# Performance work log

Hardware: AMD Instinct MI355X
Metric: run time of the kernel (lower is better)

Reference implementation:

```python
import jax, jax.numpy as jnp
import numpy as np

N_NODE = 100000
N_EDGE = 1000000
HID = 64
ATTN = 32
N_REL = 1000
N_LAYER = 2
REL_VOCAB = 2 * N_REL + 5


def setup_inputs() -> dict:
    key = jax.random.key(0)
    ks = jax.random.split(key, 16)
    sub = jax.random.randint(ks[0], (N_EDGE,), 0, N_NODE)
    rel = jax.random.randint(ks[1], (N_EDGE,), 0, REL_VOCAB)
    obj = jax.random.randint(ks[2], (N_EDGE,), 0, N_NODE)
    zero = jnp.zeros((N_EDGE,), dtype=jnp.int64 if jax.config.jax_enable_x64 else jnp.int32)
    # columns: [_, _, rel, _, sub, obj] matching edges[:,2]/[:,4]/[:,5]
    edges = jnp.stack([zero, zero, rel, zero, sub, obj], axis=1)
    s = 0.05
    return {
        "edges": edges,
        "rela_embed": jax.random.normal(ks[3], (N_LAYER, REL_VOCAB, HID), jnp.float32) * s,
        "Ws": jax.random.normal(ks[4], (N_LAYER, ATTN, HID), jnp.float32) * s,
        "Wr": jax.random.normal(ks[5], (N_LAYER, ATTN, HID), jnp.float32) * s,
        "w_alpha_w": jax.random.normal(ks[6], (N_LAYER, 1, ATTN), jnp.float32) * s,
        "w_alpha_b": jax.random.normal(ks[7], (N_LAYER, 1), jnp.float32) * s,
        "W_h": jax.random.normal(ks[8], (N_LAYER, HID, HID), jnp.float32) * s,
        "gru_Wih": jax.random.normal(ks[9], (N_LAYER, 3 * HID, HID), jnp.float32) * s,
        "gru_Whh": jax.random.normal(ks[10], (N_LAYER, 3 * HID, HID), jnp.float32) * s,
        "gru_bih": jax.random.normal(ks[11], (N_LAYER, 3 * HID), jnp.float32) * s,
        "gru_bhh": jax.random.normal(ks[12], (N_LAYER, 3 * HID), jnp.float32) * s,
        "W_final": jax.random.normal(ks[13], (HID,), jnp.float32) * s,
    }


def _gru_cell(x, h, Wih, Whh, bih, bhh):
    # PyTorch nn.GRU single step; gate order: r, z, n
    gi = x @ Wih.T + bih          # [N, 3H]
    gh = h @ Whh.T + bhh          # [N, 3H]
    gi_r, gi_z, gi_n = jnp.split(gi, 3, axis=-1)
    gh_r, gh_z, gh_n = jnp.split(gh, 3, axis=-1)
    r = jax.nn.sigmoid(gi_r + gh_r)
    z = jax.nn.sigmoid(gi_z + gh_z)
    n = jnp.tanh(gi_n + r * gh_n)
    return (1.0 - z) * n + z * h


def reference(edges, rela_embed, Ws, Wr, w_alpha_w, w_alpha_b, W_h,
              gru_Wih, gru_Whh, gru_bih, gru_bhh, W_final):
    sub = edges[:, 4]
    rel = edges[:, 2]
    obj = edges[:, 5]
    hidden = jnp.zeros((N_NODE, HID), jnp.float32)
    h0 = jnp.zeros((N_NODE, HID), jnp.float32)
    for i in range(N_LAYER):
        hs = hidden[sub]                          # [E, H] gather
        hr = rela_embed[i][rel]                   # [E, H] gather
        # attention: sigmoid(w_alpha(relu(Ws hs + Wr hr)))
        a = jax.nn.relu(hs @ Ws[i].T + hr @ Wr[i].T)       # [E, A]
        alpha = jax.nn.sigmoid(a @ w_alpha_w[i].T + w_alpha_b[i])  # [E, 1]
        message = alpha * (hs + hr)               # [E, H]
        agg = jax.ops.segment_sum(message, obj, num_segments=N_NODE)  # [N, H]
        hidden = jax.nn.relu(agg @ W_h[i].T)       # act = relu
        # dropout is identity in eval; GRU gate (seq len 1)
        h = _gru_cell(hidden, h0, gru_Wih[i], gru_Whh[i], gru_bih[i], gru_bhh[i])
        hidden = h
        h0 = h
    scores = hidden @ W_final                      # [N_NODE]
    return scores
```

## Files before the change

kernel.cpp:

```cpp
#include <hip/hip_runtime.h>

#define N_NODE 100000
#define N_PAD  100064
#define N_EDGE 1000000
#define HID 64
#define ATTN 32
#define REL_VOCAB 2005

#define CBSHIFT 9
#define CBN    512
#define NCB    196
#define MAXCB  8192
#define LCAP   6400
#define N_SLOT (NCB*MAXCB)
#define ACHUNK 4096

typedef short  bf16x8 __attribute__((ext_vector_type(8)));
typedef float  f32x4  __attribute__((ext_vector_type(4)));

__device__ __forceinline__ float sigf(float x){ return 1.0f/(1.0f+__expf(-x)); }
__device__ __forceinline__ float bf2f(unsigned short u){
  return __uint_as_float(((unsigned int)u) << 16);
}
__device__ __forceinline__ unsigned short f2bf(float f){
  unsigned int x = __float_as_uint(f);
  x += 0x7fffu + ((x >> 16) & 1u);
  return (unsigned short)(x >> 16);
}

__device__ __forceinline__ float dot64(const float4* a, const float4* __restrict__ w){
  float s0=0.f,s1=0.f,s2=0.f,s3=0.f;
  #pragma unroll
  for (int i=0;i<16;i++){
    float4 av=a[i]; float4 wv=w[i];
    s0=fmaf(av.x,wv.x,s0); s1=fmaf(av.y,wv.y,s1);
    s2=fmaf(av.z,wv.z,s2); s3=fmaf(av.w,wv.w,s3);
  }
  return (s0+s1)+(s2+s3);
}

__global__ void __launch_bounds__(256, 4) k_pre(
    const float* __restrict__ re, const float* __restrict__ Wr,
    const float* __restrict__ ww, const float* __restrict__ wb,
    unsigned short* __restrict__ srel16, unsigned short* __restrict__ re16,
    float* __restrict__ hrW1)
{
  int w = (blockIdx.x*blockDim.x + threadIdx.x) >> 6;
  int l = threadIdx.x & 63;
  if (w >= REL_VOCAB) return;
  const int r = w;
  const int j = l & 31;
  const bool hi = (l >= 32);

  float4 ev[16];
  const float4* ep = (const float4*)(re + (size_t)(hi ? REL_VOCAB + r : r)*HID);
  #pragma unroll
  for (int i=0;i<16;i++) ev[i]=ep[i];

  const float4* wrow = (const float4*)(Wr + (size_t)(hi ? ATTN + j : j)*HID);
  float d = dot64(ev, wrow);

  if (hi) hrW1[r*ATTN + j] = d;

  float p = hi ? 0.f : fmaxf(d, 0.f) * ww[j];
  p += __shfl_xor(p, 1);
  p += __shfl_xor(p, 2);
  p += __shfl_xor(p, 4);
  p += __shfl_xor(p, 8);
  p += __shfl_xor(p, 16);
  p += __shfl_xor(p, 32);
  float alpha = sigf(p + wb[0]);

  float e0l = re[(size_t)r*HID + l];
  float e1l = re[(size_t)(REL_VOCAB + r)*HID + l];
  srel16[r*HID + l] = f2bf(alpha * e0l);
  re16[r*HID + l]   = f2bf(e1l);
}

__global__ void k_izero(int* __restrict__ p, int n){
  int i = blockIdx.x*blockDim.x + threadIdx.x;
  if (i < n) p[i] = 0;
}

__global__ void k_wt(const float* __restrict__ Wh, const float* __restrict__ Wih,
                     const float* __restrict__ Whh, const float* __restrict__ Ws,
                     unsigned short* __restrict__ pkWh, unsigned short* __restrict__ pkWih,
                     unsigned short* __restrict__ pkWhh, unsigned short* __restrict__ pkWs)
{
  int tid = blockIdx.x*blockDim.x + threadIdx.x;
  if (tid >= 116*64) return;
  int rec = tid >> 6, l = tid & 63;
  const float* src; unsigned short* dst; int tile, c;
  if (rec < 16){
    int li = rec >> 3, q = rec & 7; tile = q >> 1; c = q & 1;
    src = Wh + li*4096;
    dst = pkWh + (size_t)((li*8 + q)*64 + l)*8;
  } else if (rec < 64){
    int q2 = rec - 16; int li = q2 / 24, q = q2 % 24; tile = q >> 1; c = q & 1;
    src = Wih + li*12288;
    dst = pkWih + (size_t)((li*24 + q)*64 + l)*8;
  } else if (rec < 112){
    int q2 = rec - 64; int li = q2 / 24, q = q2 % 24; tile = q >> 1; c = q & 1;
    src = Whh + li*12288;
    dst = pkWhh + (size_t)((li*24 + q)*64 + l)*8;
  } else {
    int q = rec - 112; tile = q >> 1; c = q & 1;
    src = Ws + ATTN*HID;
    dst = pkWs + (size_t)(q*64 + l)*8;
  }
  int row = tile*16 + (l&15);
  int k0  = c*32 + (l>>4)*8;
  #pragma unroll
  for (int j=0;j<8;j++) dst[j] = f2bf(src[row*64 + k0 + j]);
}

__global__ void __launch_bounds__(256, 4) k_part(
    const int* __restrict__ edges, int* __restrict__ gcursor,
    uint2* __restrict__ tmp)
{
  __shared__ int hcnt[NCB];
  __shared__ int hbase[NCB];
  __shared__ int hcur[NCB];
  const int t = threadIdx.x;
  const int base = blockIdx.x * ACHUNK;
  const int nE = min(ACHUNK, N_EDGE - base);

  if (t < NCB){ hcnt[t] = 0; }
  __syncthreads();

  unsigned pk[16]; int bb[16], lo[16];
  const int2* e2 = (const int2*)edges;
  #pragma unroll
  for (int j=0;j<16;j++){
    int idx = j*256 + t;
    if (idx < nE){
      int e = base + idx;
      int rel = e2[e*3+1].x;
      int2 so = e2[e*3+2];
      pk[j] = ((unsigned)rel << 17) | (unsigned)so.x;
      bb[j] = so.y >> CBSHIFT;
      lo[j] = so.y & (CBN-1);
      atomicAdd(&hcnt[bb[j]], 1);
    } else bb[j] = -1;
  }
  __syncthreads();
  if (t < NCB){
    hbase[t] = (hcnt[t] > 0) ? atomicAdd(&gcursor[t], hcnt[t]) : 0;
    hcur[t] = 0;
  }
  __syncthreads();
  #pragma unroll
  for (int j=0;j<16;j++){
    if (bb[j] >= 0){
      int pos = hbase[bb[j]] + atomicAdd(&hcur[bb[j]], 1);
      if (pos < MAXCB)
        tmp[(size_t)bb[j]*MAXCB + pos] = make_uint2(pk[j], (unsigned)lo[j]);
    }
  }
}

__global__ void __launch_bounds__(256, 2) k_bsort2(
    const uint2* __restrict__ tmp, const int* __restrict__ gcursor,
    unsigned int* __restrict__ pairP, int* __restrict__ startArr,
    int* __restrict__ endArr)
{
  __shared__ int lcnt[CBN];
  __shared__ int lsc[CBN];
  __shared__ int lcur[CBN];
  __shared__ unsigned int lout[LCAP];
  const int b = blockIdx.x, t = threadIdx.x;
  const int base = b*MAXCB;
  const int size = min(gcursor[b], LCAP);

  lcnt[t] = 0; lcnt[256+t] = 0;
  __syncthreads();
  for (int i=t; i<size; i+=256)
    atomicAdd(&lcnt[tmp[base+i].y], 1);
  __syncthreads();

  int cA = lcnt[t], cB = lcnt[256+t];
  lsc[t] = cA; lsc[256+t] = cB;
  __syncthreads();
  #pragma unroll
  for (int off=1; off<256; off<<=1){
    int vA = (t>=off) ? lsc[t-off] : 0;
    int vB = (t>=off) ? lsc[256+t-off] : 0;
    __syncthreads();
    lsc[t] += vA; lsc[256+t] += vB;
    __syncthreads();
  }
  int totA = lsc[255];
  __syncthreads();
  lsc[256+t] += totA;
  __syncthreads();

  {
    int inclA = lsc[t], exclA = inclA - cA;
    lcur[t] = exclA;
    int n = b*CBN + t;
    if (n < N_NODE){ startArr[n] = base + exclA; endArr[n] = base + inclA; }
    int inclB = lsc[256+t], exclB = inclB - cB;
    lcur[256+t] = exclB;
    int n2 = b*CBN + 256 + t;
    if (n2 < N_NODE){ startArr[n2] = base + exclB; endArr[n2] = base + inclB; }
  }
  __syncthreads();

  for (int i=t; i<size; i+=256){
    uint2 p = tmp[base+i];
    int pos = atomicAdd(&lcur[p.y], 1);
    lout[pos] = p.x;
  }
  __syncthreads();
  for (int i=t; i<size; i+=256)
    pairP[base+i] = lout[i];
}

__global__ void k_agg0(const int* __restrict__ startArr, const int* __restrict__ endArr,
                       const unsigned int* __restrict__ pairP,
                       const unsigned short* __restrict__ srel16,
                       unsigned short* __restrict__ agg16)
{
  int t = blockIdx.x*blockDim.x + threadIdx.x;
  int n = __builtin_amdgcn_readfirstlane(t >> 6);
  int k = t & 63;
  if (n >= N_NODE) return;
  int b = startArr[n], e_ = endArr[n];
  float acc = 0.f;
  int i = b;
  for (; i+3 < e_; i += 4){
    int r0=pairP[i]>>17, r1=pairP[i+1]>>17, r2=pairP[i+2]>>17, r3=pairP[i+3]>>17;
    float v0=bf2f(srel16[r0*HID+k]), v1=bf2f(srel16[r1*HID+k]);
    float v2=bf2f(srel16[r2*HID+k]), v3=bf2f(srel16[r3*HID+k]);
    acc += v0; acc += v1; acc += v2; acc += v3;
  }
  for (; i < e_; ++i) acc += bf2f(srel16[(pairP[i]>>17)*HID + k]);
  agg16[(size_t)n*HID + k] = f2bf(acc);
}

__global__ void __launch_bounds__(256, 4) k_alphaM(
    const unsigned int* __restrict__ pairP, const int* __restrict__ gcursor,
    const unsigned short* __restrict__ h16,
    const float* __restrict__ hrW1, const unsigned short* __restrict__ pkWs,
    const float* __restrict__ ww1, const float* __restrict__ wb1,
    float* __restrict__ alphaS)
{
  const int t = threadIdx.x;
  const int w = t >> 6, l = t & 63;
  const int lr = l & 15, lg = l >> 4;
  const int i0 = (blockIdx.x*4 + w) * 16;
  const int bkt   = i0 >> 13;
  const int local = i0 & (MAXCB-1);
  const int size  = min(gcursor[bkt], LCAP);
  if (local >= size) return;

  unsigned pe = pairP[i0 + lr];
  int subA = (int)(pe & 0x1FFFFu);
  bf16x8 a0 = *(const bf16x8*)(h16 + (size_t)subA*HID + lg*8);
  bf16x8 a1 = *(const bf16x8*)(h16 + (size_t)subA*HID + 32 + lg*8);

  bf16x8 b00 = *(const bf16x8*)(pkWs + (size_t)(0*64 + l)*8);
  bf16x8 b01 = *(const bf16x8*)(pkWs + (size_t)(1*64 + l)*8);
  bf16x8 b10 = *(const bf16x8*)(pkWs + (size_t)(2*64 + l)*8);
  bf16x8 b11 = *(const bf16x8*)(pkWs + (size_t)(3*64 + l)*8);

  f32x4 acc0 = {0.f,0.f,0.f,0.f}, acc1 = {0.f,0.f,0.f,0.f};
  acc0 = __builtin_amdgcn_mfma_f32_16x16x32_bf16(a0, b00, acc0, 0,0,0);
  acc0 = __builtin_amdgcn_mfma_f32_16x16x32_bf16(a1, b01, acc0, 0,0,0);
  acc1 = __builtin_amdgcn_mfma_f32_16x16x32_bf16(a0, b10, acc1, 0,0,0);
  acc1 = __builtin_amdgcn_mfma_f32_16x16x32_bf16(a1, b11, acc1, 0,0,0);

  float wlo = ww1[lr], whi = ww1[16 + lr];
  float bias = wb1[0];
  float s[4];
  #pragma unroll
  for (int r=0;r<4;r++){
    int e = i0 + lg*4 + r;
    int rel = (int)(pairP[e] >> 17);
    float v0 = fmaxf(acc0[r] + hrW1[rel*ATTN + lr],      0.f);
    float v1 = fmaxf(acc1[r] + hrW1[rel*ATTN + 16 + lr], 0.f);
    float p = fmaf(v0, wlo, v1*whi);
    p += __shfl_xor(p, 1);
    p += __shfl_xor(p, 2);
    p += __shfl_xor(p, 4);
    p += __shfl_xor(p, 8);
    s[r] = sigf(p + bias);
  }
  if (lr == 0)
    *(float4*)(alphaS + i0 + lg*4) = make_float4(s[0], s[1], s[2], s[3]);
}

__global__ void k_agg1(const int* __restrict__ startArr, const int* __restrict__ endArr,
                       const unsigned int* __restrict__ pairP,
                       const float* __restrict__ alphaS,
                       const unsigned short* __restrict__ h16,
                       const unsigned short* __restrict__ re16,
                       unsigned short* __restrict__ agg16)
{
  int t = blockIdx.x*blockDim.x + threadIdx.x;
  int n = __builtin_amdgcn_readfirstlane(t >> 6);
  int k = t & 63;
  if (n >= N_NODE) return;
  int b = startArr[n], e_ = endArr[n];
  float acc = 0.f;
  int i = b;
  for (; i+1 < e_; i += 2){
    unsigned p0 = pairP[i], p1 = pairP[i+1];
    int s0 = (int)(p0 & 0x1FFFFu), r0 = (int)(p0 >> 17);
    int s1 = (int)(p1 & 0x1FFFFu), r1 = (int)(p1 >> 17);
    float al0 = alphaS[i], al1 = alphaS[i+1];
    float h0 = bf2f(h16[(size_t)s0*HID + k]);
    float h1 = bf2f(h16[(size_t)s1*HID + k]);
    float v0 = bf2f(re16[r0*HID + k]);
    float v1 = bf2f(re16[r1*HID + k]);
    acc = fmaf(al0, h0 + v0, acc);
    acc = fmaf(al1, h1 + v1, acc);
  }
  if (i < e_){
    unsigned p0 = pairP[i];
    int s0 = (int)(p0 & 0x1FFFFu), r0 = (int)(p0 >> 17);
    acc = fmaf(alphaS[i], bf2f(h16[(size_t)s0*HID + k]) + bf2f(re16[r0*HID + k]), acc);
  }
  agg16[(size_t)n*HID + k] = f2bf(acc);
}

template<int HAS_H0>
__global__ void __launch_bounds__(256, 2) k_node2(
    const unsigned short* __restrict__ agg16,
    const unsigned short* __restrict__ h16,
    const unsigned short* __restrict__ pkWh,
    const unsigned short* __restrict__ pkWih,
    const unsigned short* __restrict__ pkWhh,
    const float* __restrict__ bih, const float* __restrict__ bhh,
    unsigned short* __restrict__ h16_out,
    const float* __restrict__ wf, float* __restrict__ score, int mode)
{
  __shared__ unsigned short xlds[4096];

  const int t  = threadIdx.x;
  const int w  = t >> 6, l = t & 63;
  const int lr = l & 15;
  const int lg = l >> 4;
  const int n0 = blockIdx.x * 64;
  const int rowA = n0 + w*16 + lr;

  bf16x8 aA0 = *(const bf16x8*)(agg16 + (size_t)rowA*HID + lg*8);
  bf16x8 aA1 = *(const bf16x8*)(agg16 + (size_t)rowA*HID + 32 + lg*8);
  bf16x8 hA0, hA1;
  if (HAS_H0){
    hA0 = *(const bf16x8*)(h16 + (size_t)rowA*HID + lg*8);
    hA1 = *(const bf16x8*)(h16 + (size_t)rowA*HID + 32 + lg*8);
  }

  float bir[4],biz[4],bin[4],bhr[4],bhz[4],bhn[4],wfv[4];
  #pragma unroll
  for (int nt=0;nt<4;nt++){
    int ch = nt*16 + lr;
    bir[nt]=bih[ch]; biz[nt]=bih[64+ch]; bin[nt]=bih[128+ch];
    bhr[nt]=bhh[ch]; bhz[nt]=bhh[64+ch]; bhn[nt]=bhh[128+ch];
    wfv[nt]=wf[ch];
  }

  #pragma unroll
  for (int nt=0;nt<4;nt++){
    f32x4 acc = {0.f,0.f,0.f,0.f};
    bf16x8 b0 = *(const bf16x8*)(pkWh + (size_t)((nt*2+0)*64 + l)*8);
    bf16x8 b1 = *(const bf16x8*)(pkWh + (size_t)((nt*2+1)*64 + l)*8);
    acc = __builtin_amdgcn_mfma_f32_16x16x32_bf16(aA0, b0, acc, 0,0,0);
    acc = __builtin_amdgcn_mfma_f32_16x16x32_bf16(aA1, b1, acc, 0,0,0);
    #pragma unroll
    for (int r=0;r<4;r++){
      int m = lg*4 + r, col = nt*16 + lr;
      xlds[w*1024 + m*64 + (col ^ ((m&7)<<3))] = f2bf(fmaxf(acc[r], 0.f));
    }
  }
  __syncthreads();

  const int xbase = w*1024 + lr*64;
  const int sw = (lr&7)<<3;
  bf16x8 xA0 = *(const bf16x8*)&xlds[xbase + ((lg*8)      ^ sw)];
  bf16x8 xA1 = *(const bf16x8*)&xlds[xbase + ((32 + lg*8) ^ sw)];

  float rv[16], zv[16], hv[16];
  #pragma unroll
  for (int g=0; g<2; ++g){
    #pragma unroll
    for (int nt=0;nt<4;nt++){
      int gt = g*4 + nt;
      f32x4 ai = {0.f,0.f,0.f,0.f};
      bf16x8 bi0 = *(const bf16x8*)(pkWih + (size_t)((gt*2+0)*64 + l)*8);
      bf16x8 bi1 = *(const bf16x8*)(pkWih + (size_t)((gt*2+1)*64 + l)*8);
      ai = __builtin_amdgcn_mfma_f32_16x16x32_bf16(xA0, bi0, ai, 0,0,0);
      ai = __builtin_amdgcn_mfma_f32_16x16x32_bf16(xA1, bi1, ai, 0,0,0);
      f32x4 ah = {0.f,0.f,0.f,0.f};
      if (HAS_H0){
        bf16x8 bh0 = *(const bf16x8*)(pkWhh + (size_t)((gt*2+0)*64 + l)*8);
        bf16x8 bh1 = *(const bf16x8*)(pkWhh + (size_t)((gt*2+1)*64 + l)*8);
        ah = __builtin_amdgcn_mfma_f32_16x16x32_bf16(hA0, bh0, ah, 0,0,0);
        ah = __builtin_amdgcn_mfma_f32_16x16x32_bf16(hA1, bh1, ah, 0,0,0);
      }
      #pragma unroll
      for (int r=0;r<4;r++){
        float bi_ = (g==0) ? bir[nt] : biz[nt];
        float bh_ = (g==0) ? bhr[nt] : bhz[nt];
        float v = sigf(ai[r] + bi_ + ah[r] + bh_);
        if (g==0) rv[nt*4+r] = v; else zv[nt*4+r] = v;
      }
    }
  }
  #pragma unroll
  for (int nt=0;nt<4;nt++){
    int gt = 8 + nt;
    f32x4 ai = {0.f,0.f,0.f,0.f};
    bf16x8 bi0 = *(const bf16x8*)(pkWih + (size_t)((gt*2+0)*64 + l)*8);
    bf16x8 bi1 = *(const bf16x8*)(pkWih + (size_t)((gt*2+1)*64 + l)*8);
    ai = __builtin_amdgcn_mfma_f32_16x16x32_bf16(xA0, bi0, ai, 0,0,0);
    ai = __builtin_amdgcn_mfma_f32_16x16x32_bf16(xA1, bi1, ai, 0,0,0);
    f32x4 ah = {0.f,0.f,0.f,0.f};
    if (HAS_H0){
      bf16x8 bh0 = *(const bf16x8*)(pkWhh + (size_t)((gt*2+0)*64 + l)*8);
      bf16x8 bh1 = *(const bf16x8*)(pkWhh + (size_t)((gt*2+1)*64 + l)*8);
      ah = __builtin_amdgcn_mfma_f32_16x16x32_bf16(hA0, bh0, ah, 0,0,0);
      ah = __builtin_amdgcn_mfma_f32_16x16x32_bf16(hA1, bh1, ah, 0,0,0);
    }
    #pragma unroll
    for (int r=0;r<4;r++){
      float gin = ai[r] + bin[nt];
      float ghn = ah[r] + bhn[nt];
      float rr  = rv[nt*4+r];
      float nn  = tanhf(fmaf(rr, ghn, gin));
      float z   = zv[nt*4+r];
      float h0v = 0.f;
      if (HAS_H0)
        h0v = bf2f(h16[(size_t)(n0 + w*16 + lg*4 + r)*HID + nt*16 + lr]);
      hv[nt*4+r] = (1.f - z)*nn + z*h0v;
    }
  }

  if (mode == 0){
    __syncthreads();
    #pragma unroll
    for (int nt=0;nt<4;nt++)
      #pragma unroll
      for (int r=0;r<4;r++){
        int m = lg*4 + r, col = nt*16 + lr;
        xlds[w*1024 + m*64 + (col ^ ((m&7)<<3))] = f2bf(hv[nt*4+r]);
      }
    __syncthreads();
    int rr2 = l >> 2, cc = l & 3;
    int n = n0 + w*16 + rr2;
    if (n < N_NODE){
      int base = w*1024 + rr2*64, s2 = (rr2&7)<<3;
      bf16x8 v0 = *(const bf16x8*)&xlds[base + ((cc*16)     ^ s2)];
      bf16x8 v1 = *(const bf16x8*)&xlds[base + ((cc*16 + 8) ^ s2)];
      *(bf16x8*)(h16_out + (size_t)n*HID + cc*16)     = v0;
      *(bf16x8*)(h16_out + (size_t)n*HID + cc*16 + 8) = v1;
    }
  } else {
    #pragma unroll
    for (int r=0;r<4;r++){
      float p = 0.f;
      #pragma unroll
      for (int nt=0;nt<4;nt++) p = fmaf(hv[nt*4+r], wfv[nt], p);
      p += __shfl_xor(p, 1);
      p += __shfl_xor(p, 2);
      p += __shfl_xor(p, 4);
      p += __shfl_xor(p, 8);
      if (lr == 0){
        int n = n0 + w*16 + lg*4 + r;
        if (n < N_NODE) score[n] = p;
      }
    }
  }
}

extern "C" void kernel_launch(void* const* d_in, const int* in_sizes, int n_in,
                              void* d_out, int out_size, void* d_ws, size_t ws_size,
                              hipStream_t stream)
{
  const int*   edges = (const int*)  d_in[0];
  const float* re    = (const float*)d_in[1];
  const float* Ws    = (const float*)d_in[2];
  const float* Wr    = (const float*)d_in[3];
  const float* ww    = (const float*)d_in[4];
  const float* wb    = (const float*)d_in[5];
  const float* Wh    = (const float*)d_in[6];
  const float* Wih   = (const float*)d_in[7];
  const float* Whh   = (const float*)d_in[8];
  const float* bih   = (const float*)d_in[9];
  const float* bhh   = (const float*)d_in[10];
  const float* wf    = (const float*)d_in[11];
  float* out = (float*)d_out;

  unsigned short* agg16  = (unsigned short*)d_ws;
  unsigned short* h16    = agg16 + (size_t)N_PAD*HID;
  unsigned short* srel16 = h16 + (size_t)N_PAD*HID;
  unsigned short* re16   = srel16 + REL_VOCAB*HID;
  unsigned short* pkWh   = re16 + REL_VOCAB*HID;
  unsigned short* pkWih  = pkWh  + 2*4096;
  unsigned short* pkWhh  = pkWih + 2*12288;
  unsigned short* pkWs   = pkWhh + 2*12288;
  float* hrW1      = (float*)(pkWs + 2048);
  float* alphaS    = hrW1 + REL_VOCAB*ATTN;
  uint2* tmp       = (uint2*)(alphaS + N_SLOT);
  unsigned int* pairP = (unsigned int*)(tmp + N_SLOT);
  int*   startArr  = (int*)(pairP + N_SLOT);
  int*   endArr    = startArr + NCB*CBN;
  int*   gcursor   = endArr + NCB*CBN;

  k_izero<<<1, 256, 0, stream>>>(gcursor, 256);
  k_part<<<(N_EDGE + ACHUNK - 1)/ACHUNK, 256, 0, stream>>>(edges, gcursor, tmp);
  k_bsort2<<<NCB, 256, 0, stream>>>(tmp, gcursor, pairP, startArr, endArr);

  k_pre<<<(REL_VOCAB*64+255)/256, 256, 0, stream>>>(re, Wr, ww, wb, srel16, re16, hrW1);
  k_wt<<<(116*64+255)/256, 256, 0, stream>>>(Wh, Wih, Whh, Ws, pkWh, pkWih, pkWhh, pkWs);

  const int NB_NODE2 = (N_NODE + 63) / 64;

  k_agg0<<<(N_NODE*64)/256, 256, 0, stream>>>(startArr, endArr, pairP, srel16, agg16);
  k_node2<0><<<NB_NODE2, 256, 0, stream>>>(agg16, h16,
        pkWh, pkWih, pkWhh, bih, bhh, h16, wf, out, 0);

  k_alphaM<<<N_SLOT/64, 256, 0, stream>>>(pairP, gcursor, h16, hrW1, pkWs,
        ww + ATTN, wb + 1, alphaS);
  k_agg1<<<(N_NODE*64)/256, 256, 0, stream>>>(startArr, endArr, pairP, alphaS,
        h16, re16, agg16);
  k_node2<1><<<NB_NODE2, 256, 0, stream>>>(agg16, h16,
        pkWh + 4096, pkWih + 12288, pkWhh + 12288, bih + 3*HID, bhh + 3*HID,
        h16, wf, out, 1);
}
```

Measured before the change: 203.5 us.

## Fuse layer-1 attention and aggregation into one kernel with float atomics

Merges the per-edge attention kernel and the per-node gather-aggregate into a single edge-parallel kernel. Each wave computes alpha for 16 sorted edges, accumulates messages per destination run in registers, and flushes them with float atomicAdd into a zeroed fp32 aggregate buffer. To support this, the bucket sort also writes each edge's local node id, and the node kernel gains a variant that reads the fp32 aggregate and packs it to bf16. This removes the alphaS round trip and the extra edge traversal, at the cost of a full-buffer zero pass, atomic traffic, and summation order that is no longer deterministic.

```diff
diff --git a/kernel.cpp b/kernel.cpp
--- a/kernel.cpp
+++ b/kernel.cpp
@@ -26,6 +26,14 @@
   unsigned int x = __float_as_uint(f);
   x += 0x7fffu + ((x >> 16) & 1u);
   return (unsigned short)(x >> 16);
+}
+__device__ __forceinline__ bf16x8 pk8(float4 a, float4 b){
+  bf16x8 r;
+  r[0]=(short)f2bf(a.x); r[1]=(short)f2bf(a.y);
+  r[2]=(short)f2bf(a.z); r[3]=(short)f2bf(a.w);
+  r[4]=(short)f2bf(b.x); r[5]=(short)f2bf(b.y);
+  r[6]=(short)f2bf(b.z); r[7]=(short)f2bf(b.w);
+  return r;
 }
 
 __device__ __forceinline__ float dot64(const float4* a, const float4* __restrict__ w){
@@ -80,6 +88,11 @@
 __global__ void k_izero(int* __restrict__ p, int n){
   int i = blockIdx.x*blockDim.x + threadIdx.x;
   if (i < n) p[i] = 0;
+}
+
+__global__ void k_zero4(float4* __restrict__ p, int n4){
+  int i = blockIdx.x*blockDim.x + threadIdx.x;
+  if (i < n4) p[i] = make_float4(0.f,0.f,0.f,0.f);
 }
 
 __global__ void k_wt(const float* __restrict__ Wh, const float* __restrict__ Wih,
@@ -161,13 +174,13 @@
 
 __global__ void __launch_bounds__(256, 2) k_bsort2(
     const uint2* __restrict__ tmp, const int* __restrict__ gcursor,
-    unsigned int* __restrict__ pairP, int* __restrict__ startArr,
-    int* __restrict__ endArr)
+    unsigned int* __restrict__ pairP, unsigned short* __restrict__ nodeS,
+    int* __restrict__ startArr, int* __restrict__ endArr)
 {
   __shared__ int lcnt[CBN];
   __shared__ int lsc[CBN];
   __shared__ int lcur[CBN];
-  __shared__ unsigned int lout[LCAP];
+  __shared__ uint2 lout[LCAP];
   const int b = blockIdx.x, t = threadIdx.x;
   const int base = b*MAXCB;
   const int size = min(gcursor[b], LCAP);
@@ -209,11 +222,14 @@
   for (int i=t; i<size; i+=256){
     uint2 p = tmp[base+i];
     int pos = atomicAdd(&lcur[p.y], 1);
-    lout[pos] = p.x;
-  }
-  __syncthreads();
-  for (int i=t; i<size; i+=256)
-    pairP[base+i] = lout[i];
+    lout[pos] = p;
+  }
+  __syncthreads();
+  for (int i=t; i<size; i+=256){
+    uint2 q = lout[i];
+    pairP[base+i] = q.x;
+    nodeS[base+i] = (unsigned short)q.y;
+  }
 }
 
 __global__ void k_agg0(const int* __restrict__ startArr, const int* __restrict__ endArr,
@@ -238,12 +254,12 @@
   agg16[(size_t)n*HID + k] = f2bf(acc);
 }
 
-__global__ void __launch_bounds__(256, 4) k_alphaM(
-    const unsigned int* __restrict__ pairP, const int* __restrict__ gcursor,
-    const unsigned short* __restrict__ h16,
+__global__ void __launch_bounds__(256, 4) k_fuse1(
+    const unsigned int* __restrict__ pairP, const unsigned short* __restrict__ nodeS,
+    const int* __restrict__ gcursor, const unsigned short* __restrict__ h16,
     const float* __restrict__ hrW1, const unsigned short* __restrict__ pkWs,
     const float* __restrict__ ww1, const float* __restrict__ wb1,
-    float* __restrict__ alphaS)
+    const unsigned short* __restrict__ re16, float* __restrict__ agg32)
 {
   const int t = threadIdx.x;
   const int w = t >> 6, l = t & 63;
@@ -253,8 +269,10 @@
   const int local = i0 & (MAXCB-1);
   const int size  = min(gcursor[bkt], LCAP);
   if (local >= size) return;
+  const int nv = min(16, size - local);
 
   unsigned pe = pairP[i0 + lr];
+  int ns = (int)nodeS[i0 + lr];
   int subA = (int)(pe & 0x1FFFFu);
   bf16x8 a0 = *(const bf16x8*)(h16 + (size_t)subA*HID + lg*8);
   bf16x8 a1 = *(const bf16x8*)(h16 + (size_t)subA*HID + 32 + lg*8);
@@ -275,8 +293,8 @@
   float s[4];
   #pragma unroll
   for (int r=0;r<4;r++){
-    int e = i0 + lg*4 + r;
-    int rel = (int)(pairP[e] >> 17);
+    int pe_er = __shfl((int)pe, lg*4 + r);
+    int rel = ((unsigned)pe_er) >> 17;
     float v0 = fmaxf(acc0[r] + hrW1[rel*ATTN + lr],      0.f);
     float v1 = fmaxf(acc1[r] + hrW1[rel*ATTN + 16 + lr], 0.f);
     float p = fmaf(v0, wlo, v1*whi);
@@ -286,47 +304,36 @@
     p += __shfl_xor(p, 8);
     s[r] = sigf(p + bias);
   }
-  if (lr == 0)
-    *(float4*)(alphaS + i0 + lg*4) = make_float4(s[0], s[1], s[2], s[3]);
-}
-
-__global__ void k_agg1(const int* __restrict__ startArr, const int* __restrict__ endArr,
-                       const unsigned int* __restrict__ pairP,
-                       const float* __restrict__ alphaS,
-                       const unsigned short* __restrict__ h16,
-                       const unsigned short* __restrict__ re16,
-                       unsigned short* __restrict__ agg16)
-{
-  int t = blockIdx.x*blockDim.x + threadIdx.x;
-  int n = __builtin_amdgcn_readfirstlane(t >> 6);
-  int k = t & 63;
-  if (n >= N_NODE) return;
-  int b = startArr[n], e_ = endArr[n];
+
+  const int nodeBase = bkt * CBN;
   float acc = 0.f;
-  int i = b;
-  for (; i+1 < e_; i += 2){
-    unsigned p0 = pairP[i], p1 = pairP[i+1];
-    int s0 = (int)(p0 & 0x1FFFFu), r0 = (int)(p0 >> 17);
-    int s1 = (int)(p1 & 0x1FFFFu), r1 = (int)(p1 >> 17);
-    float al0 = alphaS[i], al1 = alphaS[i+1];
-    float h0 = bf2f(h16[(size_t)s0*HID + k]);
-    float h1 = bf2f(h16[(size_t)s1*HID + k]);
-    float v0 = bf2f(re16[r0*HID + k]);
-    float v1 = bf2f(re16[r1*HID + k]);
-    acc = fmaf(al0, h0 + v0, acc);
-    acc = fmaf(al1, h1 + v1, acc);
-  }
-  if (i < e_){
-    unsigned p0 = pairP[i];
-    int s0 = (int)(p0 & 0x1FFFFu), r0 = (int)(p0 >> 17);
-    acc = fmaf(alphaS[i], bf2f(h16[(size_t)s0*HID + k]) + bf2f(re16[r0*HID + k]), acc);
-  }
-  agg16[(size_t)n*HID + k] = f2bf(acc);
-}
-
-template<int HAS_H0>
+  int prev = -1;
+  #pragma unroll
+  for (int e=0; e<16; ++e){
+    int pe_e = __shfl((int)pe, e);
+    int ns_e = __shfl(ns, e);
+    float al = __shfl(s[e & 3], (e >> 2) * 16);
+    if (e < nv){
+      int sub_e = pe_e & 0x1FFFF;
+      int rel_e = ((unsigned)pe_e) >> 17;
+      float hv = bf2f(h16[(size_t)sub_e*HID + l]);
+      float rv = bf2f(re16[rel_e*HID + l]);
+      if (ns_e != prev){
+        if (prev >= 0)
+          atomicAdd(&agg32[(size_t)(nodeBase + prev)*HID + l], acc);
+        acc = 0.f;
+        prev = ns_e;
+      }
+      acc = fmaf(al, hv + rv, acc);
+    }
+  }
+  if (prev >= 0)
+    atomicAdd(&agg32[(size_t)(nodeBase + prev)*HID + l], acc);
+}
+
+template<int HAS_H0, int AGGF32>
 __global__ void __launch_bounds__(256, 2) k_node2(
-    const unsigned short* __restrict__ agg16,
+    const void* __restrict__ aggP,
     const unsigned short* __restrict__ h16,
     const unsigned short* __restrict__ pkWh,
     const unsigned short* __restrict__ pkWih,
@@ -344,8 +351,17 @@
   const int n0 = blockIdx.x * 64;
   const int rowA = n0 + w*16 + lr;
 
-  bf16x8 aA0 = *(const bf16x8*)(agg16 + (size_t)rowA*HID + lg*8);
-  bf16x8 aA1 = *(const bf16x8*)(agg16 + (size_t)rowA*HID + 32 + lg*8);
+  bf16x8 aA0, aA1;
+  if (AGGF32){
+    const float4* ap = (const float4*)((const float*)aggP + (size_t)rowA*HID);
+    float4 u0 = ap[lg*2], u1 = ap[lg*2+1];
+    float4 u2 = ap[8+lg*2], u3 = ap[9+lg*2];
+    aA0 = pk8(u0, u1); aA1 = pk8(u2, u3);
+  } else {
+    const unsigned short* a16 = (const unsigned short*)aggP;
+    aA0 = *(const bf16x8*)(a16 + (size_t)rowA*HID + lg*8);
+    aA1 = *(const bf16x8*)(a16 + (size_t)rowA*HID + 32 + lg*8);
+  }
   bf16x8 hA0, hA1;
   if (HAS_H0){
     hA0 = *(const bf16x8*)(h16 + (size_t)rowA*HID + lg*8);
@@ -501,16 +517,19 @@
   unsigned short* pkWhh  = pkWih + 2*12288;
   unsigned short* pkWs   = pkWhh + 2*12288;
   float* hrW1      = (float*)(pkWs + 2048);
-  float* alphaS    = hrW1 + REL_VOCAB*ATTN;
-  uint2* tmp       = (uint2*)(alphaS + N_SLOT);
+  float* agg32     = hrW1 + REL_VOCAB*ATTN;
+  uint2* tmp       = (uint2*)(agg32 + (size_t)N_PAD*HID);
   unsigned int* pairP = (unsigned int*)(tmp + N_SLOT);
-  int*   startArr  = (int*)(pairP + N_SLOT);
+  unsigned short* nodeS = (unsigned short*)(pairP + N_SLOT);
+  int*   startArr  = (int*)(nodeS + N_SLOT);
   int*   endArr    = startArr + NCB*CBN;
   int*   gcursor   = endArr + NCB*CBN;
 
   k_izero<<<1, 256, 0, stream>>>(gcursor, 256);
+  k_zero4<<<((N_PAD*HID/4) + 255)/256, 256, 0, stream>>>((float4*)agg32, N_PAD*HID/4);
+
   k_part<<<(N_EDGE + ACHUNK - 1)/ACHUNK, 256, 0, stream>>>(edges, gcursor, tmp);
-  k_bsort2<<<NCB, 256, 0, stream>>>(tmp, gcursor, pairP, startArr, endArr);
+  k_bsort2<<<NCB, 256, 0, stream>>>(tmp, gcursor, pairP, nodeS, startArr, endArr);
 
   k_pre<<<(REL_VOCAB*64+255)/256, 256, 0, stream>>>(re, Wr, ww, wb, srel16, re16, hrW1);
   k_wt<<<(116*64+255)/256, 256, 0, stream>>>(Wh, Wih, Whh, Ws, pkWh, pkWih, pkWhh, pkWs);
@@ -518,14 +537,12 @@
   const int NB_NODE2 = (N_NODE + 63) / 64;
 
   k_agg0<<<(N_NODE*64)/256, 256, 0, stream>>>(startArr, endArr, pairP, srel16, agg16);
-  k_node2<0><<<NB_NODE2, 256, 0, stream>>>(agg16, h16,
+  k_node2<0,0><<<NB_NODE2, 256, 0, stream>>>(agg16, h16,
         pkWh, pkWih, pkWhh, bih, bhh, h16, wf, out, 0);
 
-  k_alphaM<<<N_SLOT/64, 256, 0, stream>>>(pairP, gcursor, h16, hrW1, pkWs,
-        ww + ATTN, wb + 1, alphaS);
-  k_agg1<<<(N_NODE*64)/256, 256, 0, stream>>>(startArr, endArr, pairP, alphaS,
-        h16, re16, agg16);
-  k_node2<1><<<NB_NODE2, 256, 0, stream>>>(agg16, h16,
+  k_fuse1<<<N_SLOT/64, 256, 0, stream>>>(pairP, nodeS, gcursor, h16, hrW1, pkWs,
+        ww + ATTN, wb + 1, re16, agg32);
+  k_node2<1,1><<<NB_NODE2, 256, 0, stream>>>(agg32, h16,
         pkWh + 4096, pkWih + 12288, pkWhh + 12288, bih + 3*HID, bhh + 3*HID,
         h16, wf, out, 1);
 }
```

Result: slower. 219.6 us (+7.9%).

## Fuse layer-2 attention scoring into per-node aggregation kernel

Applied to the files above, without the earlier changes.

Merges the MFMA-based attention-alpha kernel with the per-destination aggregation kernel: each wave owns one node, computes alphas for 16 incoming edges at a time with MFMA, and immediately accumulates alpha*(h+rel) via shuffles. This removes the alphaS buffer round-trip and one kernel launch. In exchange, MFMA tiles become partially empty for nodes with fewer than 16 edges (about 10 on average), which wastes matrix work. Reads past the node's edge range also pull in neighbouring entries and their h16 rows, though only for alpha computation that is then masked.

```diff
diff --git a/kernel.cpp b/kernel.cpp
--- a/kernel.cpp
+++ b/kernel.cpp
@@ -238,90 +238,72 @@
   agg16[(size_t)n*HID + k] = f2bf(acc);
 }
 
-__global__ void __launch_bounds__(256, 4) k_alphaM(
-    const unsigned int* __restrict__ pairP, const int* __restrict__ gcursor,
+__global__ void __launch_bounds__(256, 4) k_fuse2(
+    const int* __restrict__ startArr, const int* __restrict__ endArr,
+    const unsigned int* __restrict__ pairP,
     const unsigned short* __restrict__ h16,
     const float* __restrict__ hrW1, const unsigned short* __restrict__ pkWs,
     const float* __restrict__ ww1, const float* __restrict__ wb1,
-    float* __restrict__ alphaS)
+    const unsigned short* __restrict__ re16,
+    unsigned short* __restrict__ agg16)
 {
   const int t = threadIdx.x;
   const int w = t >> 6, l = t & 63;
   const int lr = l & 15, lg = l >> 4;
-  const int i0 = (blockIdx.x*4 + w) * 16;
-  const int bkt   = i0 >> 13;
-  const int local = i0 & (MAXCB-1);
-  const int size  = min(gcursor[bkt], LCAP);
-  if (local >= size) return;
-
-  unsigned pe = pairP[i0 + lr];
-  int subA = (int)(pe & 0x1FFFFu);
-  bf16x8 a0 = *(const bf16x8*)(h16 + (size_t)subA*HID + lg*8);
-  bf16x8 a1 = *(const bf16x8*)(h16 + (size_t)subA*HID + 32 + lg*8);
+  const int n = __builtin_amdgcn_readfirstlane(blockIdx.x*4 + w);
+  if (n >= N_NODE) return;
+  const int b = startArr[n], e_ = endArr[n];
 
   bf16x8 b00 = *(const bf16x8*)(pkWs + (size_t)(0*64 + l)*8);
   bf16x8 b01 = *(const bf16x8*)(pkWs + (size_t)(1*64 + l)*8);
   bf16x8 b10 = *(const bf16x8*)(pkWs + (size_t)(2*64 + l)*8);
   bf16x8 b11 = *(const bf16x8*)(pkWs + (size_t)(3*64 + l)*8);
-
-  f32x4 acc0 = {0.f,0.f,0.f,0.f}, acc1 = {0.f,0.f,0.f,0.f};
-  acc0 = __builtin_amdgcn_mfma_f32_16x16x32_bf16(a0, b00, acc0, 0,0,0);
-  acc0 = __builtin_amdgcn_mfma_f32_16x16x32_bf16(a1, b01, acc0, 0,0,0);
-  acc1 = __builtin_amdgcn_mfma_f32_16x16x32_bf16(a0, b10, acc1, 0,0,0);
-  acc1 = __builtin_amdgcn_mfma_f32_16x16x32_bf16(a1, b11, acc1, 0,0,0);
-
-  float wlo = ww1[lr], whi = ww1[16 + lr];
-  float bias = wb1[0];
-  float s[4];
-  #pragma unroll
-  for (int r=0;r<4;r++){
-    int e = i0 + lg*4 + r;
-    int rel = (int)(pairP[e] >> 17);
-    float v0 = fmaxf(acc0[r] + hrW1[rel*ATTN + lr],      0.f);
-    float v1 = fmaxf(acc1[r] + hrW1[rel*ATTN + 16 + lr], 0.f);
-    float p = fmaf(v0, wlo, v1*whi);
-    p += __shfl_xor(p, 1);
-    p += __shfl_xor(p, 2);
-    p += __shfl_xor(p, 4);
-    p += __shfl_xor(p, 8);
-    s[r] = sigf(p + bias);
-  }
-  if (lr == 0)
-    *(float4*)(alphaS + i0 + lg*4) = make_float4(s[0], s[1], s[2], s[3]);
-}
-
-__global__ void k_agg1(const int* __restrict__ startArr, const int* __restrict__ endArr,
-                       const unsigned int* __restrict__ pairP,
-                       const float* __restrict__ alphaS,
-                       const unsigned short* __restrict__ h16,
-                       const unsigned short* __restrict__ re16,
-                       unsigned short* __restrict__ agg16)
-{
-  int t = blockIdx.x*blockDim.x + threadIdx.x;
-  int n = __builtin_amdgcn_readfirstlane(t >> 6);
-  int k = t & 63;
-  if (n >= N_NODE) return;
-  int b = startArr[n], e_ = endArr[n];
+  const float wlo = ww1[lr], whi = ww1[16 + lr];
+  const float bias = wb1[0];
+
   float acc = 0.f;
-  int i = b;
-  for (; i+1 < e_; i += 2){
-    unsigned p0 = pairP[i], p1 = pairP[i+1];
-    int s0 = (int)(p0 & 0x1FFFFu), r0 = (int)(p0 >> 17);
-    int s1 = (int)(p1 & 0x1FFFFu), r1 = (int)(p1 >> 17);
-    float al0 = alphaS[i], al1 = alphaS[i+1];
-    float h0 = bf2f(h16[(size_t)s0*HID + k]);
-    float h1 = bf2f(h16[(size_t)s1*HID + k]);
-    float v0 = bf2f(re16[r0*HID + k]);
-    float v1 = bf2f(re16[r1*HID + k]);
-    acc = fmaf(al0, h0 + v0, acc);
-    acc = fmaf(al1, h1 + v1, acc);
-  }
-  if (i < e_){
-    unsigned p0 = pairP[i];
-    int s0 = (int)(p0 & 0x1FFFFu), r0 = (int)(p0 >> 17);
-    acc = fmaf(alphaS[i], bf2f(h16[(size_t)s0*HID + k]) + bf2f(re16[r0*HID + k]), acc);
-  }
-  agg16[(size_t)n*HID + k] = f2bf(acc);
+  for (int c = b; c < e_; c += 16){
+    const int nv = e_ - c;
+
+    unsigned pe = pairP[c + lr];
+    int subA = (int)(pe & 0x1FFFFu);
+    bf16x8 a0 = *(const bf16x8*)(h16 + (size_t)subA*HID + lg*8);
+    bf16x8 a1 = *(const bf16x8*)(h16 + (size_t)subA*HID + 32 + lg*8);
+
+    f32x4 acc0 = {0.f,0.f,0.f,0.f}, acc1 = {0.f,0.f,0.f,0.f};
+    acc0 = __builtin_amdgcn_mfma_f32_16x16x32_bf16(a0, b00, acc0, 0,0,0);
+    acc0 = __builtin_amdgcn_mfma_f32_16x16x32_bf16(a1, b01, acc0, 0,0,0);
+    acc1 = __builtin_amdgcn_mfma_f32_16x16x32_bf16(a0, b10, acc1, 0,0,0);
+    acc1 = __builtin_amdgcn_mfma_f32_16x16x32_bf16(a1, b11, acc1, 0,0,0);
+
+    float s[4];
+    #pragma unroll
+    for (int r=0;r<4;r++){
+      int pe_er = __shfl((int)pe, lg*4 + r);
+      int rel = ((unsigned)pe_er) >> 17;
+      float v0 = fmaxf(acc0[r] + hrW1[rel*ATTN + lr],      0.f);
+      float v1 = fmaxf(acc1[r] + hrW1[rel*ATTN + 16 + lr], 0.f);
+      float p = fmaf(v0, wlo, v1*whi);
+      p += __shfl_xor(p, 1);
+      p += __shfl_xor(p, 2);
+      p += __shfl_xor(p, 4);
+      p += __shfl_xor(p, 8);
+      s[r] = sigf(p + bias);
+    }
+
+    #pragma unroll
+    for (int e=0; e<16; ++e){
+      if (e >= nv) break;
+      int pe_e = __shfl((int)pe, e);
+      float al = __shfl(s[e & 3], (e >> 2) * 16);
+      int sub_e = pe_e & 0x1FFFF;
+      int rel_e = ((unsigned)pe_e) >> 17;
+      float hv = bf2f(h16[(size_t)sub_e*HID + l]);
+      float rv = bf2f(re16[rel_e*HID + l]);
+      acc = fmaf(al, hv + rv, acc);
+    }
+  }
+  agg16[(size_t)n*HID + l] = f2bf(acc);
 }
 
 template<int HAS_H0>
@@ -501,8 +483,7 @@
   unsigned short* pkWhh  = pkWih + 2*12288;
   unsigned short* pkWs   = pkWhh + 2*12288;
   float* hrW1      = (float*)(pkWs + 2048);
-  float* alphaS    = hrW1 + REL_VOCAB*ATTN;
-  uint2* tmp       = (uint2*)(alphaS + N_SLOT);
+  uint2* tmp       = (uint2*)(hrW1 + REL_VOCAB*ATTN);
   unsigned int* pairP = (unsigned int*)(tmp + N_SLOT);
   int*   startArr  = (int*)(pairP + N_SLOT);
   int*   endArr    = startArr + NCB*CBN;
@@ -521,10 +502,8 @@
   k_node2<0><<<NB_NODE2, 256, 0, stream>>>(agg16, h16,
         pkWh, pkWih, pkWhh, bih, bhh, h16, wf, out, 0);
 
-  k_alphaM<<<N_SLOT/64, 256, 0, stream>>>(pairP, gcursor, h16, hrW1, pkWs,
-        ww + ATTN, wb + 1, alphaS);
-  k_agg1<<<(N_NODE*64)/256, 256, 0, stream>>>(startArr, endArr, pairP, alphaS,
-        h16, re16, agg16);
+  k_fuse2<<<(N_NODE*64)/256, 256, 0, stream>>>(startArr, endArr, pairP,
+        h16, hrW1, pkWs, ww + ATTN, wb + 1, re16, agg16);
   k_node2<1><<<NB_NODE2, 256, 0, stream>>>(agg16, h16,
         pkWh + 4096, pkWih + 12288, pkWhh + 12288, bih + 3*HID, bhh + 3*HID,
         h16, wf, out, 1);
```

New measurement: 202.5 us. No clear change (-0.5%).
